# Optimization experiments

Measured on AMD Instinct MI355X. Metric: run time of the kernel, lower is better.

## Reference

```python
import jax, jax.numpy as jnp
import numpy as np

D = 8       # latent dim d
NE = 4      # n_emb
NS = 3      # n_outer stages
NI = 5      # n_inner iterations per stage
EPS = 1e-5  # LayerNorm eps
TAU = 1.0   # route_tau (default), max(1.0, 1e-3) = 1.0


def _ln(x, g, b):
    m = x.mean(-1, keepdims=True)
    v = ((x - m) ** 2).mean(-1, keepdims=True)
    return (x - m) / jnp.sqrt(v + EPS) * g + b


def _inner(E, u, Bm, Wp, bp, W1, b1, W2, b2):
    # E: [B, NE, D], u: [B, D]
    Bsz = E.shape[0]
    # bilinear interaction: outer product e_i u^T + B_i, for all i at once
    M = E[:, :, :, None] * u[:, None, None, :] + Bm[None]      # [B, NE, D, D]
    H = M.reshape(Bsz, NE, D * D) @ Wp.T + bp                  # W_proj: [B, NE, D]
    # softmax routing: s_i = softmax(route(h_i)/tau) over experts
    lg = jax.nn.relu(H @ W1.T + b1) @ W2.T + b2                # [B, NE, NE]
    s = jax.nn.softmax(lg / TAU, axis=-1)
    mix = jnp.einsum('bne,bed->bnd', s, H)                     # per-i mixture of H
    return E + mix


def setup_inputs() -> dict:
    B = 131072
    key = jax.random.key(0)
    ks = jax.random.split(key, 32)
    f32 = jnp.float32
    inp = {
        'cl':     jax.random.normal(ks[0], (B,), f32),
        'cd':     jax.random.normal(ks[1], (B,), f32),
        're_log': jax.random.normal(ks[2], (B,), f32),
        'mach':   jax.random.normal(ks[3], (B,), f32),
        'alpha':  jax.random.normal(ks[4], (B,), f32),
        'u':      jax.random.normal(ks[5], (B, D), f32),
        'We':    jax.random.normal(ks[6], (NE, D, 2), f32) * 0.5,
        'be':    jnp.zeros((NE, D), f32),
        # per-stage InnerBlockAblated params (stacked over NS stages)
        'Bmat':  jax.random.normal(ks[7], (NS, NE, D, D), f32) * 0.05,
        'Wproj': jax.random.normal(ks[8], (NS, D, D * D), f32) * 0.1,
        'bproj': jnp.zeros((NS, D), f32),
        'Wr1':   jax.random.normal(ks[9], (NS, D, D), f32) * 0.3,
        'br1':   jnp.zeros((NS, D), f32),
        'Wr2':   jax.random.normal(ks[10], (NS, NE, D), f32) * 0.3,
        'br2':   jnp.zeros((NS, NE), f32),
        # post-stage LayerNorm
        'ln_g':  jnp.ones((D,), f32),
        'ln_b':  jnp.zeros((D,), f32),
        # final mixing over embeddings: Linear(n_emb*d, n_emb)
        'Wout':  jax.random.normal(ks[11], (NE, NE * D), f32) * 0.1,
        'bout':  jnp.zeros((NE,), f32),
        # final LayerNorm
        'fg':    jnp.ones((D,), f32),
        'fb':    jnp.zeros((D,), f32),
        # heads: head_cst Linear(d, 18), head_cl Linear(d, 1)
        'Wcst':  jax.random.normal(ks[12], (18, D), f32) * 0.2,
        'bcst':  jnp.zeros((18,), f32),
        'Wcl':   jax.random.normal(ks[13], (1, D), f32) * 0.2,
        'bcl':   jnp.zeros((1,), f32),
    }
    return inp


def reference(cl, cd, re_log, mach, alpha, u, We, be, Bmat, Wproj, bproj,
              Wr1, br1, Wr2, br2, ln_g, ln_b, Wout, bout, fg, fb,
              Wcst, bcst, Wcl, bcl):
    # _stack_pairs: [B, 4, 2]
    pairs = jnp.stack([
        jnp.stack([cl, alpha], -1),
        jnp.stack([cd, alpha], -1),
        jnp.stack([re_log, alpha], -1),
        jnp.stack([mach, alpha], -1),
    ], axis=1)
    # embed: per-embedding Linear(2, d) + Tanh  -> E: [B, NE, D]
    E = jnp.tanh(jnp.einsum('bne,nde->bnd', pairs, We) + be[None])
    # outer stages: n_inner inner blocks each, then post-stage LayerNorm
    for s_idx in range(NS):
        for _ in range(NI):
            E = _inner(E, u, Bmat[s_idx], Wproj[s_idx], bproj[s_idx],
                       Wr1[s_idx], br1[s_idx], Wr2[s_idx], br2[s_idx])
        E = _ln(E, ln_g, ln_b)
    # final softmax mixing over embeddings (w_out_logits)
    Bsz = E.shape[0]
    w = jax.nn.softmax(E.reshape(Bsz, NE * D) @ Wout.T + bout, axis=-1)  # [B, NE]
    z = _ln(jnp.einsum('bn,bnd->bd', w, E), fg, fb)                       # [B, D]
    # heads, concatenated: [B, 18 + 1]
    return jnp.concatenate([z @ Wcst.T + bcst, z @ Wcl.T + bcl], axis=-1)
```

## Files before the change

### kernel.cpp

```cpp
#include <hip/hip_runtime.h>

#define D 8
#define NE 4
#define NS 3
#define NI 5
#define LN_EPS 1e-5f

#define STAGE_STRIDE 144
#define SOFF_W1  0
#define SOFF_W2T 64
#define SOFF_C   96
#define SOFF_B1  128
#define SOFF_B2  136
#define OFF_WP   432
#define OFF_LN   1968
#define WLDS_SIZE 1984

typedef float f2 __attribute__((ext_vector_type(2)));
typedef float f4 __attribute__((ext_vector_type(4)));

__device__ __forceinline__ f2 max2(f2 a, f2 b) { return __builtin_elementwise_max(a, b); }
__device__ __forceinline__ f2 bc(float s) { return (f2){s, s}; }

__device__ __forceinline__ void pk_fma_lo(f2& acc, f2 a, f2 b) {
    asm("v_pk_fma_f32 %0, %1, %2, %0 op_sel:[0,0,0] op_sel_hi:[1,0,1]"
        : "+v"(acc) : "v"(a), "v"(b));
}
__device__ __forceinline__ void pk_fma_hi(f2& acc, f2 a, f2 b) {
    asm("v_pk_fma_f32 %0, %1, %2, %0 op_sel:[0,1,0] op_sel_hi:[1,1,1]"
        : "+v"(acc) : "v"(a), "v"(b));
}
__device__ __forceinline__ void pk_fma_ee(f2& acc, f2 a, f2 b) {
    asm("v_pk_fma_f32 %0, %1, %2, %0"
        : "+v"(acc) : "v"(a), "v"(b));
}

__global__ void precompute_C_kernel(const float* __restrict__ Bmat,
                                    const float* __restrict__ Wproj,
                                    const float* __restrict__ bproj,
                                    float* __restrict__ C) {
    int idx = threadIdx.x;
    if (idx >= NS * NE * D) return;
    int s = idx / (NE * D);
    int rem = idx % (NE * D);
    int n = rem / D;
    int d = rem % D;
    const float* bm = Bmat + ((size_t)s * NE + n) * 64;
    const float* wp = Wproj + ((size_t)s * D + d) * 64;
    float acc = bproj[s * D + d];
    #pragma unroll
    for (int k = 0; k < 64; ++k) acc += bm[k] * wp[k];
    C[s * 32 + ((n >> 1) * 8 + d) * 2 + (n & 1)] = acc;
}

__device__ __forceinline__ float fast_tanh(float x) {
    float e = __expf(2.f * x);
    return 1.f - 2.f * __builtin_amdgcn_rcpf(e + 1.f);
}

__device__ __forceinline__ f4 ld4(const float* p) {
    return *reinterpret_cast<const f4*>(p);
}

__global__ __launch_bounds__(256, 2) void whisp_kernel(
    const float* __restrict__ cl, const float* __restrict__ cd,
    const float* __restrict__ re_log, const float* __restrict__ mach,
    const float* __restrict__ alpha, const float* __restrict__ u,
    const float* __restrict__ We, const float* __restrict__ be,
    const float* __restrict__ Wproj,
    const float* __restrict__ Wr1, const float* __restrict__ br1,
    const float* __restrict__ Wr2, const float* __restrict__ br2,
    const float* __restrict__ ln_g, const float* __restrict__ ln_b,
    const float* __restrict__ Wout, const float* __restrict__ bout,
    const float* __restrict__ fg, const float* __restrict__ fb,
    const float* __restrict__ Wcst, const float* __restrict__ bcst,
    const float* __restrict__ Wcl, const float* __restrict__ bcl,
    const float* __restrict__ Cpre,
    float* __restrict__ out, int B)
{
    __shared__ __align__(16) float wlds[WLDS_SIZE];
    __shared__ __align__(16) f4 ubuf[2 * 256];
    __shared__ float souts[256 * 19];

    const int tid = threadIdx.x;
    const int row0 = blockIdx.x * 256 + tid;
    const bool active = (row0 < B);
    const int row = active ? row0 : (B - 1);

    for (int i = tid; i < NS * 64; i += 256) {
        int s = i / 64, j = i % 64;
        wlds[s * STAGE_STRIDE + SOFF_W1 + j] = Wr1[i];
    }
    for (int i = tid; i < NS * 32; i += 256) {
        int s = i / 32, j = i % 32, d = j / 4, e = j % 4;
        wlds[s * STAGE_STRIDE + SOFF_W2T + j] = Wr2[s * 32 + e * 8 + d];
    }
    for (int i = tid; i < NS * 32; i += 256) {
        int s = i / 32, j = i % 32;
        wlds[s * STAGE_STRIDE + SOFF_C + j] = Cpre[i];
    }
    for (int i = tid; i < NS * 8; i += 256) {
        int s = i / 8, j = i % 8;
        wlds[s * STAGE_STRIDE + SOFF_B1 + j] = br1[i];
    }
    for (int i = tid; i < NS * 4; i += 256) {
        int s = i / 4, j = i % 4;
        wlds[s * STAGE_STRIDE + SOFF_B2 + j] = br2[i];
    }
    for (int i = tid; i < 1536; i += 256) wlds[OFF_WP + i] = Wproj[i];
    for (int i = tid; i < 8; i += 256) { wlds[OFF_LN + i] = ln_g[i]; wlds[OFF_LN + 8 + i] = ln_b[i]; }

    {
        const f4* up = reinterpret_cast<const f4*>(u + (size_t)row * D);
        ubuf[tid]       = up[0];
        ubuf[256 + tid] = up[1];
    }
    float xs[NE] = { cl[row], cd[row], re_log[row], mach[row] };
    float al = alpha[row];

    f2 E2[2][D];
    #pragma unroll
    for (int nn = 0; nn < 2; ++nn) {
        #pragma unroll
        for (int d = 0; d < D; ++d) {
            int na = 2 * nn, nb = 2 * nn + 1;
            float pa = We[na * 16 + d * 2] * xs[na] + We[na * 16 + d * 2 + 1] * al + be[na * D + d];
            float pb = We[nb * 16 + d * 2] * xs[nb] + We[nb * 16 + d * 2 + 1] * al + be[nb * D + d];
            E2[nn][d] = (f2){ fast_tanh(pa), fast_tanh(pb) };
        }
    }

    __syncthreads();

    int zero = 0;

    #pragma unroll 1
    for (int s = 0; s < NS; ++s) {
        const float* stage_base = wlds + s * STAGE_STRIDE;

        f2 tp[D][4];
        {
            f4 uq0 = ubuf[tid], uq1 = ubuf[256 + tid];
            f2 uu2[4] = { uq0.lo, uq0.hi, uq1.lo, uq1.hi };
            const float* Wp = wlds + OFF_WP + s * 512;
            #pragma unroll
            for (int d = 0; d < D; ++d) {
                #pragma unroll
                for (int kp = 0; kp < 4; ++kp) {
                    int i0 = 2 * kp, i1 = 2 * kp + 1;
                    f4 a0 = ld4(Wp + d * 64 + i0 * 8);
                    f4 a1 = ld4(Wp + d * 64 + i0 * 8 + 4);
                    f4 b0 = ld4(Wp + d * 64 + i1 * 8);
                    f4 b1 = ld4(Wp + d * 64 + i1 * 8 + 4);
                    f2 accA = uu2[0] * a0.lo;
                    pk_fma_ee(accA, uu2[1], a0.hi);
                    pk_fma_ee(accA, uu2[2], a1.lo);
                    pk_fma_ee(accA, uu2[3], a1.hi);
                    f2 accB = uu2[0] * b0.lo;
                    pk_fma_ee(accB, uu2[1], b0.hi);
                    pk_fma_ee(accB, uu2[2], b1.lo);
                    pk_fma_ee(accB, uu2[3], b1.hi);
                    tp[d][kp] = (f2){ accA.x + accA.y, accB.x + accB.y };
                }
            }
        }

        #pragma unroll 1
        for (int it = 0; it < NI; ++it) {
            asm volatile("" : "+v"(zero));
            const float* sb = stage_base + zero;

            f2 H2[2][D];
            #pragma unroll
            for (int nn = 0; nn < 2; ++nn) {
                #pragma unroll
                for (int dp = 0; dp < 4; ++dp) {
                    f4 cq = ld4(sb + SOFF_C + nn * 16 + dp * 4);
                    H2[nn][2 * dp]     = cq.lo;
                    H2[nn][2 * dp + 1] = cq.hi;
                }
            }
            #pragma unroll
            for (int d = 0; d < D; ++d) {
                #pragma unroll
                for (int nn = 0; nn < 2; ++nn) {
                    f2 acc = H2[nn][d];
                    pk_fma_lo(acc, E2[nn][0], tp[d][0]);
                    pk_fma_hi(acc, E2[nn][1], tp[d][0]);
                    pk_fma_lo(acc, E2[nn][2], tp[d][1]);
                    pk_fma_hi(acc, E2[nn][3], tp[d][1]);
                    pk_fma_lo(acc, E2[nn][4], tp[d][2]);
                    pk_fma_hi(acc, E2[nn][5], tp[d][2]);
                    pk_fma_lo(acc, E2[nn][6], tp[d][3]);
                    pk_fma_hi(acc, E2[nn][7], tp[d][3]);
                    H2[nn][d] = acc;
                }
            }

            f2 lg2[2][NE];
            {
                float b20 = sb[SOFF_B2 + 0], b21 = sb[SOFF_B2 + 1];
                float b22 = sb[SOFF_B2 + 2], b23 = sb[SOFF_B2 + 3];
                #pragma unroll
                for (int nn = 0; nn < 2; ++nn) {
                    lg2[nn][0] = bc(b20); lg2[nn][1] = bc(b21);
                    lg2[nn][2] = bc(b22); lg2[nn][3] = bc(b23);
                }
            }

            #pragma unroll
            for (int d = 0; d < D; ++d) {
                f4 wa = ld4(sb + SOFF_W1 + d * 8);
                f4 wb = ld4(sb + SOFF_W1 + d * 8 + 4);
                f4 w2 = ld4(sb + SOFF_W2T + d * 4);
                float b1d = sb[SOFF_B1 + d];
                #pragma unroll
                for (int nn = 0; nn < 2; ++nn) {
                    f2 acc = bc(b1d);
                    pk_fma_lo(acc, H2[nn][0], wa.lo);
                    pk_fma_hi(acc, H2[nn][1], wa.lo);
                    pk_fma_lo(acc, H2[nn][2], wa.hi);
                    pk_fma_hi(acc, H2[nn][3], wa.hi);
                    pk_fma_lo(acc, H2[nn][4], wb.lo);
                    pk_fma_hi(acc, H2[nn][5], wb.lo);
                    pk_fma_lo(acc, H2[nn][6], wb.hi);
                    pk_fma_hi(acc, H2[nn][7], wb.hi);
                    f2 r2 = max2(acc, bc(0.f));
                    pk_fma_lo(lg2[nn][0], r2, w2.lo);
                    pk_fma_hi(lg2[nn][1], r2, w2.lo);
                    pk_fma_lo(lg2[nn][2], r2, w2.hi);
                    pk_fma_hi(lg2[nn][3], r2, w2.hi);
                }
            }

            f2 sm2[2][NE];
            #pragma unroll
            for (int nn = 0; nn < 2; ++nn) {
                f2 m2 = max2(max2(lg2[nn][0], lg2[nn][1]), max2(lg2[nn][2], lg2[nn][3]));
                f2 ee[NE];
                #pragma unroll
                for (int e = 0; e < NE; ++e) {
                    f2 tt = lg2[nn][e] - m2;
                    ee[e] = (f2){ __expf(tt.x), __expf(tt.y) };
                }
                f2 s2 = (ee[0] + ee[1]) + (ee[2] + ee[3]);
                f2 inv2 = (f2){ __builtin_amdgcn_rcpf(s2.x), __builtin_amdgcn_rcpf(s2.y) };
                #pragma unroll
                for (int e = 0; e < NE; ++e) sm2[nn][e] = ee[e] * inv2;
            }

            #pragma unroll
            for (int d = 0; d < D; ++d) {
                #pragma unroll
                for (int nn = 0; nn < 2; ++nn) {
                    f2 acc = E2[nn][d];
                    pk_fma_lo(acc, sm2[nn][0], H2[0][d]);
                    pk_fma_hi(acc, sm2[nn][1], H2[0][d]);
                    pk_fma_lo(acc, sm2[nn][2], H2[1][d]);
                    pk_fma_hi(acc, sm2[nn][3], H2[1][d]);
                    E2[nn][d] = acc;
                }
            }
        }

        float lngv[8], lnbv[8];
        {
            f4 g0 = ld4(wlds + OFF_LN),     g1 = ld4(wlds + OFF_LN + 4);
            f4 b0 = ld4(wlds + OFF_LN + 8), b1 = ld4(wlds + OFF_LN + 12);
            lngv[0]=g0.x; lngv[1]=g0.y; lngv[2]=g0.z; lngv[3]=g0.w;
            lngv[4]=g1.x; lngv[5]=g1.y; lngv[6]=g1.z; lngv[7]=g1.w;
            lnbv[0]=b0.x; lnbv[1]=b0.y; lnbv[2]=b0.z; lnbv[3]=b0.w;
            lnbv[4]=b1.x; lnbv[5]=b1.y; lnbv[6]=b1.z; lnbv[7]=b1.w;
        }
        #pragma unroll
        for (int nn = 0; nn < 2; ++nn) {
            f2 s2 = (E2[nn][0] + E2[nn][1]) + (E2[nn][2] + E2[nn][3]);
            s2 = s2 + (E2[nn][4] + E2[nn][5]) + (E2[nn][6] + E2[nn][7]);
            f2 m2 = s2 * bc(0.125f);
            f2 v2 = bc(0.f);
            #pragma unroll
            for (int d = 0; d < D; ++d) { f2 c = E2[nn][d] - m2; pk_fma_ee(v2, c, c); }
            v2 = v2 * bc(0.125f);
            f2 inv2 = (f2){ __builtin_amdgcn_rsqf(v2.x + LN_EPS),
                            __builtin_amdgcn_rsqf(v2.y + LN_EPS) };
            #pragma unroll
            for (int d = 0; d < D; ++d) {
                f2 r = bc(lnbv[d]);
                pk_fma_ee(r, (E2[nn][d] - m2) * inv2, bc(lngv[d]));
                E2[nn][d] = r;
            }
        }
    }

    float lgf[NE];
    #pragma unroll
    for (int e = 0; e < NE; ++e) {
        float a0 = bout[e], a1 = 0.f;
        #pragma unroll
        for (int d = 0; d < D; ++d) {
            a0 = fmaf(E2[0][d].x, Wout[e * 32 + 0 * D + d], a0);
            a1 = fmaf(E2[0][d].y, Wout[e * 32 + 1 * D + d], a1);
            a0 = fmaf(E2[1][d].x, Wout[e * 32 + 2 * D + d], a0);
            a1 = fmaf(E2[1][d].y, Wout[e * 32 + 3 * D + d], a1);
        }
        lgf[e] = a0 + a1;
    }
    float mx = fmaxf(fmaxf(lgf[0], lgf[1]), fmaxf(lgf[2], lgf[3]));
    float w0 = __expf(lgf[0] - mx), w1 = __expf(lgf[1] - mx);
    float w2 = __expf(lgf[2] - mx), w3 = __expf(lgf[3] - mx);
    float winv = __builtin_amdgcn_rcpf((w0 + w1) + (w2 + w3));
    w0 *= winv; w1 *= winv; w2 *= winv; w3 *= winv;

    float z[D];
    #pragma unroll
    for (int d = 0; d < D; ++d) {
        float a0 = w0 * E2[0][d].x;
        float a1 = w1 * E2[0][d].y;
        a0 = fmaf(w2, E2[1][d].x, a0);
        a1 = fmaf(w3, E2[1][d].y, a1);
        z[d] = a0 + a1;
    }
    float zm = 0.f;
    #pragma unroll
    for (int d = 0; d < D; ++d) zm += z[d];
    zm *= (1.f / D);
    float zv = 0.f;
    #pragma unroll
    for (int d = 0; d < D; ++d) { float c = z[d] - zm; zv = fmaf(c, c, zv); }
    zv *= (1.f / D);
    float zinv = __builtin_amdgcn_rsqf(zv + LN_EPS);
    #pragma unroll
    for (int d = 0; d < D; ++d)
        z[d] = (z[d] - zm) * zinv * fg[d] + fb[d];

    float zout[19];
    #pragma unroll
    for (int k = 0; k < 18; ++k) {
        float a0 = bcst[k], a1 = 0.f;
        #pragma unroll
        for (int d = 0; d < D; d += 2) {
            a0 = fmaf(z[d],     Wcst[k * D + d],     a0);
            a1 = fmaf(z[d + 1], Wcst[k * D + d + 1], a1);
        }
        zout[k] = a0 + a1;
    }
    {
        float a0 = bcl[0], a1 = 0.f;
        #pragma unroll
        for (int d = 0; d < D; d += 2) {
            a0 = fmaf(z[d],     Wcl[d],     a0);
            a1 = fmaf(z[d + 1], Wcl[d + 1], a1);
        }
        zout[18] = a0 + a1;
    }

    if (active) {
        #pragma unroll
        for (int k = 0; k < 19; ++k) souts[tid * 19 + k] = zout[k];
    }
    __syncthreads();

    const int base = blockIdx.x * 256;
    int nrows = B - base;
    if (nrows > 256) nrows = 256;
    if (nrows > 0) {
        const int cnt = nrows * 19;
        for (int i = tid; i < cnt; i += 256)
            out[(size_t)base * 19 + i] = souts[i];
    }
}

extern "C" void kernel_launch(void* const* d_in, const int* in_sizes, int n_in,
                              void* d_out, int out_size, void* d_ws, size_t ws_size,
                              hipStream_t stream) {
    const float* cl     = (const float*)d_in[0];
    const float* cd     = (const float*)d_in[1];
    const float* re_log = (const float*)d_in[2];
    const float* mach   = (const float*)d_in[3];
    const float* alpha  = (const float*)d_in[4];
    const float* u      = (const float*)d_in[5];
    const float* We     = (const float*)d_in[6];
    const float* be     = (const float*)d_in[7];
    const float* Bmat   = (const float*)d_in[8];
    const float* Wproj  = (const float*)d_in[9];
    const float* bproj  = (const float*)d_in[10];
    const float* Wr1    = (const float*)d_in[11];
    const float* br1    = (const float*)d_in[12];
    const float* Wr2    = (const float*)d_in[13];
    const float* br2    = (const float*)d_in[14];
    const float* ln_g   = (const float*)d_in[15];
    const float* ln_b   = (const float*)d_in[16];
    const float* Wout   = (const float*)d_in[17];
    const float* bout   = (const float*)d_in[18];
    const float* fg     = (const float*)d_in[19];
    const float* fb     = (const float*)d_in[20];
    const float* Wcst   = (const float*)d_in[21];
    const float* bcst   = (const float*)d_in[22];
    const float* Wcl    = (const float*)d_in[23];
    const float* bcl    = (const float*)d_in[24];

    float* Cpre = (float*)d_ws;
    const int B = in_sizes[0];

    hipLaunchKernelGGL(precompute_C_kernel, dim3(1), dim3(128), 0, stream,
                       Bmat, Wproj, bproj, Cpre);

    const int blocks = (B + 255) / 256;
    hipLaunchKernelGGL(whisp_kernel, dim3(blocks), dim3(256), 0, stream,
                       cl, cd, re_log, mach, alpha, u, We, be, Wproj,
                       Wr1, br1, Wr2, br2, ln_g, ln_b, Wout, bout, fg, fb,
                       Wcst, bcst, Wcl, bcl, Cpre, (float*)d_out, B);
}
```

Baseline: 63.84 us.

## Split each row across two lanes with DPP exchange of expert halves

Each batch row is now handled by a pair of adjacent lanes, each owning two of the four embeddings. Cross-expert mixing and the final reductions exchange partial values with DPP quad-permute moves instead of keeping all experts in one thread. Router weights and biases are re-laid out per lane parity in LDS, and the grid doubles to 128 rows per block. The aim is to halve per-thread register pressure and serial work for more parallelism, at the cost of duplicated tp/u-projection and router-weight work per lane plus extra DPP traffic.

```diff
diff --git a/kernel.cpp b/kernel.cpp
--- a/kernel.cpp
+++ b/kernel.cpp
@@ -6,15 +6,15 @@
 #define NI 5
 #define LN_EPS 1e-5f
 
-#define STAGE_STRIDE 144
+#define STAGE_STRIDE 176
 #define SOFF_W1  0
-#define SOFF_W2T 64
-#define SOFF_C   96
-#define SOFF_B1  128
-#define SOFF_B2  136
-#define OFF_WP   432
-#define OFF_LN   1968
-#define WLDS_SIZE 1984
+#define SOFF_W2P 64
+#define SOFF_C   128
+#define SOFF_B1  160
+#define SOFF_B2P 168
+#define OFF_WP   528
+#define OFF_LN   2064
+#define WLDS_SIZE 2080
 
 typedef float f2 __attribute__((ext_vector_type(2)));
 typedef float f4 __attribute__((ext_vector_type(4)));
@@ -34,6 +34,13 @@
     asm("v_pk_fma_f32 %0, %1, %2, %0"
         : "+v"(acc) : "v"(a), "v"(b));
 }
+
+__device__ __forceinline__ float xor1f(float x) {
+    int i = __builtin_bit_cast(int, x);
+    i = __builtin_amdgcn_mov_dpp(i, 0xB1, 0xF, 0xF, true);
+    return __builtin_bit_cast(float, i);
+}
+__device__ __forceinline__ f2 xor1f2(f2 x) { return (f2){ xor1f(x.x), xor1f(x.y) }; }
 
 __global__ void precompute_C_kernel(const float* __restrict__ Bmat,
                                     const float* __restrict__ Wproj,
@@ -79,21 +86,25 @@
     float* __restrict__ out, int B)
 {
     __shared__ __align__(16) float wlds[WLDS_SIZE];
-    __shared__ __align__(16) f4 ubuf[2 * 256];
-    __shared__ float souts[256 * 19];
+    __shared__ __align__(16) f4 ubuf[2 * 128];
+    __shared__ float souts[128 * 19];
 
     const int tid = threadIdx.x;
-    const int row0 = blockIdx.x * 256 + tid;
+    const int p   = tid & 1;
+    const int rl  = tid >> 1;
+    const int row0 = blockIdx.x * 128 + rl;
     const bool active = (row0 < B);
     const int row = active ? row0 : (B - 1);
+    const int eb  = 2 * p;
 
     for (int i = tid; i < NS * 64; i += 256) {
         int s = i / 64, j = i % 64;
         wlds[s * STAGE_STRIDE + SOFF_W1 + j] = Wr1[i];
     }
-    for (int i = tid; i < NS * 32; i += 256) {
-        int s = i / 32, j = i % 32, d = j / 4, e = j % 4;
-        wlds[s * STAGE_STRIDE + SOFF_W2T + j] = Wr2[s * 32 + e * 8 + d];
+    for (int i = tid; i < NS * 64; i += 256) {
+        int s = i / 64, j = i % 64, pp = j / 32, r = j % 32, d = r / 4, jj = r % 4;
+        int e = (jj < 2) ? (2 * pp + jj) : (2 * (1 - pp) + (jj - 2));
+        wlds[s * STAGE_STRIDE + SOFF_W2P + j] = Wr2[s * 32 + e * 8 + d];
     }
     for (int i = tid; i < NS * 32; i += 256) {
         int s = i / 32, j = i % 32;
@@ -103,31 +114,28 @@
         int s = i / 8, j = i % 8;
         wlds[s * STAGE_STRIDE + SOFF_B1 + j] = br1[i];
     }
-    for (int i = tid; i < NS * 4; i += 256) {
-        int s = i / 4, j = i % 4;
-        wlds[s * STAGE_STRIDE + SOFF_B2 + j] = br2[i];
+    for (int i = tid; i < NS * 8; i += 256) {
+        int s = i / 8, j = i % 8, pp = j / 4, jj = j % 4;
+        int e = (jj < 2) ? (2 * pp + jj) : (2 * (1 - pp) + (jj - 2));
+        wlds[s * STAGE_STRIDE + SOFF_B2P + j] = br2[s * 4 + e];
     }
     for (int i = tid; i < 1536; i += 256) wlds[OFF_WP + i] = Wproj[i];
     for (int i = tid; i < 8; i += 256) { wlds[OFF_LN + i] = ln_g[i]; wlds[OFF_LN + 8 + i] = ln_b[i]; }
 
     {
         const f4* up = reinterpret_cast<const f4*>(u + (size_t)row * D);
-        ubuf[tid]       = up[0];
-        ubuf[256 + tid] = up[1];
-    }
-    float xs[NE] = { cl[row], cd[row], re_log[row], mach[row] };
+        ubuf[p * 128 + rl] = up[p];
+    }
+    float xa = (p ? re_log : cl)[row];
+    float xb = (p ? mach   : cd)[row];
     float al = alpha[row];
 
-    f2 E2[2][D];
+    f2 E2[D];
     #pragma unroll
-    for (int nn = 0; nn < 2; ++nn) {
-        #pragma unroll
-        for (int d = 0; d < D; ++d) {
-            int na = 2 * nn, nb = 2 * nn + 1;
-            float pa = We[na * 16 + d * 2] * xs[na] + We[na * 16 + d * 2 + 1] * al + be[na * D + d];
-            float pb = We[nb * 16 + d * 2] * xs[nb] + We[nb * 16 + d * 2 + 1] * al + be[nb * D + d];
-            E2[nn][d] = (f2){ fast_tanh(pa), fast_tanh(pb) };
-        }
+    for (int d = 0; d < D; ++d) {
+        float pa = We[eb * 16 + d * 2] * xa + We[eb * 16 + d * 2 + 1] * al + be[eb * 8 + d];
+        float pb = We[(eb + 1) * 16 + d * 2] * xb + We[(eb + 1) * 16 + d * 2 + 1] * al + be[(eb + 1) * 8 + d];
+        E2[d] = (f2){ fast_tanh(pa), fast_tanh(pb) };
     }
 
     __syncthreads();
@@ -140,7 +148,7 @@
 
         f2 tp[D][4];
         {
-            f4 uq0 = ubuf[tid], uq1 = ubuf[256 + tid];
+            f4 uq0 = ubuf[rl], uq1 = ubuf[128 + rl];
             f2 uu2[4] = { uq0.lo, uq0.hi, uq1.lo, uq1.hi };
             const float* Wp = wlds + OFF_WP + s * 512;
             #pragma unroll
@@ -170,96 +178,82 @@
             asm volatile("" : "+v"(zero));
             const float* sb = stage_base + zero;
 
-            f2 H2[2][D];
-            #pragma unroll
-            for (int nn = 0; nn < 2; ++nn) {
-                #pragma unroll
-                for (int dp = 0; dp < 4; ++dp) {
-                    f4 cq = ld4(sb + SOFF_C + nn * 16 + dp * 4);
-                    H2[nn][2 * dp]     = cq.lo;
-                    H2[nn][2 * dp + 1] = cq.hi;
-                }
-            }
-            #pragma unroll
-            for (int d = 0; d < D; ++d) {
-                #pragma unroll
-                for (int nn = 0; nn < 2; ++nn) {
-                    f2 acc = H2[nn][d];
-                    pk_fma_lo(acc, E2[nn][0], tp[d][0]);
-                    pk_fma_hi(acc, E2[nn][1], tp[d][0]);
-                    pk_fma_lo(acc, E2[nn][2], tp[d][1]);
-                    pk_fma_hi(acc, E2[nn][3], tp[d][1]);
-                    pk_fma_lo(acc, E2[nn][4], tp[d][2]);
-                    pk_fma_hi(acc, E2[nn][5], tp[d][2]);
-                    pk_fma_lo(acc, E2[nn][6], tp[d][3]);
-                    pk_fma_hi(acc, E2[nn][7], tp[d][3]);
-                    H2[nn][d] = acc;
-                }
-            }
-
-            f2 lg2[2][NE];
+            f2 H2[D];
+            #pragma unroll
+            for (int dp = 0; dp < 4; ++dp) {
+                f4 cq = ld4(sb + SOFF_C + p * 16 + dp * 4);
+                H2[2 * dp]     = cq.lo;
+                H2[2 * dp + 1] = cq.hi;
+            }
+            #pragma unroll
+            for (int d = 0; d < D; ++d) {
+                f2 acc = H2[d];
+                pk_fma_lo(acc, E2[0], tp[d][0]);
+                pk_fma_hi(acc, E2[1], tp[d][0]);
+                pk_fma_lo(acc, E2[2], tp[d][1]);
+                pk_fma_hi(acc, E2[3], tp[d][1]);
+                pk_fma_lo(acc, E2[4], tp[d][2]);
+                pk_fma_hi(acc, E2[5], tp[d][2]);
+                pk_fma_lo(acc, E2[6], tp[d][3]);
+                pk_fma_hi(acc, E2[7], tp[d][3]);
+                H2[d] = acc;
+            }
+
+            f2 lg2[NE];
             {
-                float b20 = sb[SOFF_B2 + 0], b21 = sb[SOFF_B2 + 1];
-                float b22 = sb[SOFF_B2 + 2], b23 = sb[SOFF_B2 + 3];
-                #pragma unroll
-                for (int nn = 0; nn < 2; ++nn) {
-                    lg2[nn][0] = bc(b20); lg2[nn][1] = bc(b21);
-                    lg2[nn][2] = bc(b22); lg2[nn][3] = bc(b23);
-                }
+                f4 b2q = ld4(sb + SOFF_B2P + p * 4);
+                lg2[0] = bc(b2q.x); lg2[1] = bc(b2q.y);
+                lg2[2] = bc(b2q.z); lg2[3] = bc(b2q.w);
             }
 
             #pragma unroll
             for (int d = 0; d < D; ++d) {
                 f4 wa = ld4(sb + SOFF_W1 + d * 8);
                 f4 wb = ld4(sb + SOFF_W1 + d * 8 + 4);
-                f4 w2 = ld4(sb + SOFF_W2T + d * 4);
+                f4 w2 = ld4(sb + SOFF_W2P + p * 32 + d * 4);
                 float b1d = sb[SOFF_B1 + d];
-                #pragma unroll
-                for (int nn = 0; nn < 2; ++nn) {
-                    f2 acc = bc(b1d);
-                    pk_fma_lo(acc, H2[nn][0], wa.lo);
-                    pk_fma_hi(acc, H2[nn][1], wa.lo);
-                    pk_fma_lo(acc, H2[nn][2], wa.hi);
-                    pk_fma_hi(acc, H2[nn][3], wa.hi);
-                    pk_fma_lo(acc, H2[nn][4], wb.lo);
-                    pk_fma_hi(acc, H2[nn][5], wb.lo);
-                    pk_fma_lo(acc, H2[nn][6], wb.hi);
-                    pk_fma_hi(acc, H2[nn][7], wb.hi);
-                    f2 r2 = max2(acc, bc(0.f));
-                    pk_fma_lo(lg2[nn][0], r2, w2.lo);
-                    pk_fma_hi(lg2[nn][1], r2, w2.lo);
-                    pk_fma_lo(lg2[nn][2], r2, w2.hi);
-                    pk_fma_hi(lg2[nn][3], r2, w2.hi);
-                }
-            }
-
-            f2 sm2[2][NE];
-            #pragma unroll
-            for (int nn = 0; nn < 2; ++nn) {
-                f2 m2 = max2(max2(lg2[nn][0], lg2[nn][1]), max2(lg2[nn][2], lg2[nn][3]));
-                f2 ee[NE];
-                #pragma unroll
-                for (int e = 0; e < NE; ++e) {
-                    f2 tt = lg2[nn][e] - m2;
-                    ee[e] = (f2){ __expf(tt.x), __expf(tt.y) };
-                }
-                f2 s2 = (ee[0] + ee[1]) + (ee[2] + ee[3]);
+                f2 acc = bc(b1d);
+                pk_fma_lo(acc, H2[0], wa.lo);
+                pk_fma_hi(acc, H2[1], wa.lo);
+                pk_fma_lo(acc, H2[2], wa.hi);
+                pk_fma_hi(acc, H2[3], wa.hi);
+                pk_fma_lo(acc, H2[4], wb.lo);
+                pk_fma_hi(acc, H2[5], wb.lo);
+                pk_fma_lo(acc, H2[6], wb.hi);
+                pk_fma_hi(acc, H2[7], wb.hi);
+                f2 r2 = max2(acc, bc(0.f));
+                pk_fma_lo(lg2[0], r2, w2.lo);
+                pk_fma_hi(lg2[1], r2, w2.lo);
+                pk_fma_lo(lg2[2], r2, w2.hi);
+                pk_fma_hi(lg2[3], r2, w2.hi);
+            }
+
+            f2 sm2[NE];
+            {
+                f2 m2 = max2(max2(lg2[0], lg2[1]), max2(lg2[2], lg2[3]));
+                f2 e0 = lg2[0] - m2, e1 = lg2[1] - m2, e2 = lg2[2] - m2, e3 = lg2[3] - m2;
+                f2 x0 = (f2){ __expf(e0.x), __expf(e0.y) };
+                f2 x1 = (f2){ __expf(e1.x), __expf(e1.y) };
+                f2 x2 = (f2){ __expf(e2.x), __expf(e2.y) };
+                f2 x3 = (f2){ __expf(e3.x), __expf(e3.y) };
+                f2 s2 = (x0 + x1) + (x2 + x3);
                 f2 inv2 = (f2){ __builtin_amdgcn_rcpf(s2.x), __builtin_amdgcn_rcpf(s2.y) };
-                #pragma unroll
-                for (int e = 0; e < NE; ++e) sm2[nn][e] = ee[e] * inv2;
-            }
-
-            #pragma unroll
-            for (int d = 0; d < D; ++d) {
-                #pragma unroll
-                for (int nn = 0; nn < 2; ++nn) {
-                    f2 acc = E2[nn][d];
-                    pk_fma_lo(acc, sm2[nn][0], H2[0][d]);
-                    pk_fma_hi(acc, sm2[nn][1], H2[0][d]);
-                    pk_fma_lo(acc, sm2[nn][2], H2[1][d]);
-                    pk_fma_hi(acc, sm2[nn][3], H2[1][d]);
-                    E2[nn][d] = acc;
-                }
+                sm2[0] = x0 * inv2; sm2[1] = x1 * inv2;
+                sm2[2] = x2 * inv2; sm2[3] = x3 * inv2;
+            }
+
+            f2 Ho2[D];
+            #pragma unroll
+            for (int d = 0; d < D; ++d) Ho2[d] = xor1f2(H2[d]);
+
+            #pragma unroll
+            for (int d = 0; d < D; ++d) {
+                f2 acc = E2[d];
+                pk_fma_lo(acc, sm2[0], H2[d]);
+                pk_fma_hi(acc, sm2[1], H2[d]);
+                pk_fma_lo(acc, sm2[2], Ho2[d]);
+                pk_fma_hi(acc, sm2[3], Ho2[d]);
+                E2[d] = acc;
             }
         }
 
@@ -272,97 +266,99 @@
             lnbv[0]=b0.x; lnbv[1]=b0.y; lnbv[2]=b0.z; lnbv[3]=b0.w;
             lnbv[4]=b1.x; lnbv[5]=b1.y; lnbv[6]=b1.z; lnbv[7]=b1.w;
         }
-        #pragma unroll
-        for (int nn = 0; nn < 2; ++nn) {
-            f2 s2 = (E2[nn][0] + E2[nn][1]) + (E2[nn][2] + E2[nn][3]);
-            s2 = s2 + (E2[nn][4] + E2[nn][5]) + (E2[nn][6] + E2[nn][7]);
+        {
+            f2 s2 = (E2[0] + E2[1]) + (E2[2] + E2[3]);
+            s2 = s2 + (E2[4] + E2[5]) + (E2[6] + E2[7]);
             f2 m2 = s2 * bc(0.125f);
             f2 v2 = bc(0.f);
             #pragma unroll
-            for (int d = 0; d < D; ++d) { f2 c = E2[nn][d] - m2; pk_fma_ee(v2, c, c); }
+            for (int d = 0; d < D; ++d) { f2 c = E2[d] - m2; pk_fma_ee(v2, c, c); }
             v2 = v2 * bc(0.125f);
             f2 inv2 = (f2){ __builtin_amdgcn_rsqf(v2.x + LN_EPS),
                             __builtin_amdgcn_rsqf(v2.y + LN_EPS) };
             #pragma unroll
             for (int d = 0; d < D; ++d) {
                 f2 r = bc(lnbv[d]);
-                pk_fma_ee(r, (E2[nn][d] - m2) * inv2, bc(lngv[d]));
-                E2[nn][d] = r;
-            }
-        }
-    }
-
-    float lgf[NE];
-    #pragma unroll
-    for (int e = 0; e < NE; ++e) {
-        float a0 = bout[e], a1 = 0.f;
+                pk_fma_ee(r, (E2[d] - m2) * inv2, bc(lngv[d]));
+                E2[d] = r;
+            }
+        }
+    }
+
+    float w0, w1, w2, w3;
+    {
+        float lgf[NE];
+        #pragma unroll
+        for (int e = 0; e < NE; ++e) {
+            float a0 = 0.f, a1 = 0.f;
+            #pragma unroll
+            for (int d = 0; d < D; ++d) {
+                a0 = fmaf(E2[d].x, Wout[e * 32 + eb * 8 + d],     a0);
+                a1 = fmaf(E2[d].y, Wout[e * 32 + eb * 8 + 8 + d], a1);
+            }
+            float part = a0 + a1;
+            lgf[e] = part + xor1f(part) + bout[e];
+        }
+        float mx = fmaxf(fmaxf(lgf[0], lgf[1]), fmaxf(lgf[2], lgf[3]));
+        w0 = __expf(lgf[0] - mx); w1 = __expf(lgf[1] - mx);
+        w2 = __expf(lgf[2] - mx); w3 = __expf(lgf[3] - mx);
+        float winv = __builtin_amdgcn_rcpf((w0 + w1) + (w2 + w3));
+        w0 *= winv; w1 *= winv; w2 *= winv; w3 *= winv;
+    }
+
+    float z[D];
+    {
+        float wo0 = p ? w2 : w0;
+        float wo1 = p ? w3 : w1;
         #pragma unroll
         for (int d = 0; d < D; ++d) {
-            a0 = fmaf(E2[0][d].x, Wout[e * 32 + 0 * D + d], a0);
-            a1 = fmaf(E2[0][d].y, Wout[e * 32 + 1 * D + d], a1);
-            a0 = fmaf(E2[1][d].x, Wout[e * 32 + 2 * D + d], a0);
-            a1 = fmaf(E2[1][d].y, Wout[e * 32 + 3 * D + d], a1);
-        }
-        lgf[e] = a0 + a1;
-    }
-    float mx = fmaxf(fmaxf(lgf[0], lgf[1]), fmaxf(lgf[2], lgf[3]));
-    float w0 = __expf(lgf[0] - mx), w1 = __expf(lgf[1] - mx);
-    float w2 = __expf(lgf[2] - mx), w3 = __expf(lgf[3] - mx);
-    float winv = __builtin_amdgcn_rcpf((w0 + w1) + (w2 + w3));
-    w0 *= winv; w1 *= winv; w2 *= winv; w3 *= winv;
-
-    float z[D];
-    #pragma unroll
-    for (int d = 0; d < D; ++d) {
-        float a0 = w0 * E2[0][d].x;
-        float a1 = w1 * E2[0][d].y;
-        a0 = fmaf(w2, E2[1][d].x, a0);
-        a1 = fmaf(w3, E2[1][d].y, a1);
-        z[d] = a0 + a1;
-    }
-    float zm = 0.f;
-    #pragma unroll
-    for (int d = 0; d < D; ++d) zm += z[d];
-    zm *= (1.f / D);
-    float zv = 0.f;
-    #pragma unroll
-    for (int d = 0; d < D; ++d) { float c = z[d] - zm; zv = fmaf(c, c, zv); }
-    zv *= (1.f / D);
-    float zinv = __builtin_amdgcn_rsqf(zv + LN_EPS);
-    #pragma unroll
-    for (int d = 0; d < D; ++d)
-        z[d] = (z[d] - zm) * zinv * fg[d] + fb[d];
-
-    float zout[19];
-    #pragma unroll
-    for (int k = 0; k < 18; ++k) {
-        float a0 = bcst[k], a1 = 0.f;
-        #pragma unroll
-        for (int d = 0; d < D; d += 2) {
-            a0 = fmaf(z[d],     Wcst[k * D + d],     a0);
-            a1 = fmaf(z[d + 1], Wcst[k * D + d + 1], a1);
-        }
-        zout[k] = a0 + a1;
+            float zp = fmaf(wo0, E2[d].x, wo1 * E2[d].y);
+            z[d] = zp + xor1f(zp);
+        }
     }
     {
-        float a0 = bcl[0], a1 = 0.f;
-        #pragma unroll
-        for (int d = 0; d < D; d += 2) {
-            a0 = fmaf(z[d],     Wcl[d],     a0);
-            a1 = fmaf(z[d + 1], Wcl[d + 1], a1);
-        }
-        zout[18] = a0 + a1;
+        float zm = 0.f;
+        #pragma unroll
+        for (int d = 0; d < D; ++d) zm += z[d];
+        zm *= (1.f / D);
+        float zv = 0.f;
+        #pragma unroll
+        for (int d = 0; d < D; ++d) { float c = z[d] - zm; zv = fmaf(c, c, zv); }
+        zv *= (1.f / D);
+        float zinv = __builtin_amdgcn_rsqf(zv + LN_EPS);
+        #pragma unroll
+        for (int d = 0; d < D; ++d)
+            z[d] = (z[d] - zm) * zinv * fg[d] + fb[d];
     }
 
     if (active) {
         #pragma unroll
-        for (int k = 0; k < 19; ++k) souts[tid * 19 + k] = zout[k];
-    }
+        for (int j = 0; j < 9; ++j) {
+            int k = 2 * j + p;
+            float a0 = bcst[k], a1 = 0.f;
+            #pragma unroll
+            for (int d = 0; d < D; d += 2) {
+                a0 = fmaf(z[d],     Wcst[k * D + d],     a0);
+                a1 = fmaf(z[d + 1], Wcst[k * D + d + 1], a1);
+            }
+            souts[rl * 19 + k] = a0 + a1;
+        }
+        if (p == 0) {
+            float a0 = bcl[0], a1 = 0.f;
+            #pragma unroll
+            for (int d = 0; d < D; d += 2) {
+                a0 = fmaf(z[d],     Wcl[d],     a0);
+                a1 = fmaf(z[d + 1], Wcl[d + 1], a1);
+            }
+            souts[rl * 19 + 18] = a0 + a1;
+        }
+    }
+
     __syncthreads();
 
-    const int base = blockIdx.x * 256;
+    const int base = blockIdx.x * 128;
     int nrows = B - base;
-    if (nrows > 256) nrows = 256;
+    if (nrows > 128) nrows = 128;
     if (nrows > 0) {
         const int cnt = nrows * 19;
         for (int i = tid; i < cnt; i += 256)
@@ -405,7 +401,7 @@
     hipLaunchKernelGGL(precompute_C_kernel, dim3(1), dim3(128), 0, stream,
                        Bmat, Wproj, bproj, Cpre);
 
-    const int blocks = (B + 255) / 256;
+    const int blocks = (B + 127) / 128;
     hipLaunchKernelGGL(whisp_kernel, dim3(blocks), dim3(256), 0, stream,
                        cl, cd, re_log, mach, alpha, u, We, be, Wproj,
                        Wr1, br1, Wr2, br2, ln_g, ln_b, Wout, bout, fg, fb,
```

Result: slower. 74.15 us (+16.1%).
